# Performance work log

Hardware: AMD Instinct MI355X
Metric: run time of the kernel (lower is better)

The kernel has to match this reference:

```python
import jax, jax.numpy as jnp
import numpy as np

N = 10000
E = 160000
HEADS = 4
HC = 32      # hidden_channels
OC = 64      # out_channels
NG = 16      # n_goods
H1, H2 = 512, 256
NEG_SLOPE = 0.2


def setup_inputs() -> dict:
    key = jax.random.key(0)
    ks = jax.random.split(key, 32)
    rn = lambda k, s, sc=0.05: (jax.random.normal(k, s, jnp.float32) * sc)
    inp = {
        "x": jax.random.normal(ks[0], (N, 63), jnp.float32),
        "next_demand": jax.random.normal(ks[1], (N, 1), jnp.float32),
        "edge_index": jax.random.randint(ks[2], (2, E), 0, N),
        "eps": jax.random.normal(ks[3], (E, NG), jnp.float32),
        "Wl3": rn(ks[4], (HEADS * HC, 64)), "Wr3": rn(ks[5], (HEADS * HC, 64)),
        "att3": rn(ks[6], (HEADS, HC)), "b3": rn(ks[7], (HEADS * HC,)),
        # gat4: 128 -> 64, 1 head, mean
        "Wl4": rn(ks[8], (OC, HEADS * HC)), "Wr4": rn(ks[9], (OC, HEADS * HC)),
        "att4": rn(ks[10], (1, OC)), "b4": rn(ks[11], (OC,)),
        "Wl1": rn(ks[12], (HEADS * HC, OC)), "Wr1": rn(ks[13], (HEADS * HC, OC)),
        "att1": rn(ks[14], (HEADS, HC)), "b1": rn(ks[15], (HEADS * HC,)),
        # gat2: 128 -> 64, 1 head, mean
        "Wl2": rn(ks[16], (OC, HEADS * HC)), "Wr2": rn(ks[17], (OC, HEADS * HC)),
        "att2": rn(ks[18], (1, OC)), "b2": rn(ks[19], (OC,)),
        # MLP head: 256 -> 512 -> 256 -> n_goods (mu, std)
        "W_fc": rn(ks[20], (H1, OC * 4)), "b_fc": rn(ks[21], (H1,)),
        "W_fc1": rn(ks[22], (H2, H1)), "b_fc1": rn(ks[23], (H2,)),
        "W_mu": rn(ks[24], (NG, H2)), "b_mu": rn(ks[25], (NG,)),
        "W_std": rn(ks[26], (NG, H2)), "b_std": rn(ks[27], (NG,)),
    }
    return inp


def gatv2(x, src, dst, n, Wl, Wr, att, bias, heads, oc, concat):
    # GATv2Conv: e = a . LeakyReLU(Wl x_src + Wr x_dst), softmax over dst neighborhoods
    xl = (x @ Wl.T).reshape(n, heads, oc)
    xr = (x @ Wr.T).reshape(n, heads, oc)
    e = jax.nn.leaky_relu(xl[src] + xr[dst], NEG_SLOPE)        # [E', H, C]
    score = jnp.einsum('ehc,hc->eh', e, att)                   # [E', H]
    m = jax.ops.segment_max(score, dst, num_segments=n)        # stable segment softmax
    ex = jnp.exp(score - m[dst])
    den = jax.ops.segment_sum(ex, dst, num_segments=n)
    alpha = ex / (den[dst] + 1e-16)
    out = jax.ops.segment_sum(alpha[:, :, None] * xl[src], dst, num_segments=n)
    out = out.reshape(n, heads * oc) if concat else out.mean(axis=1)
    return out + bias


def reference(x, next_demand, edge_index, eps,
              Wl3, Wr3, att3, b3, Wl4, Wr4, att4, b4,
              Wl1, Wr1, att1, b1, Wl2, Wr2, att2, b2,
              W_fc, b_fc, W_fc1, b_fc1, W_mu, b_mu, W_std, b_std):
    n = x.shape[0]
    lrelu = lambda v: jax.nn.leaky_relu(v, NEG_SLOPE)
    loop = jnp.arange(n)
    # forward edges + self loops (PyG GATv2Conv add_self_loops=True)
    src = jnp.concatenate([edge_index[0], loop])
    dst = jnp.concatenate([edge_index[1], loop])
    # reverse edges + self loops
    rsrc = jnp.concatenate([edge_index[1], loop])
    rdst = jnp.concatenate([edge_index[0], loop])

    h = jnp.concatenate([x, next_demand.reshape(n, -1)], axis=1)   # [N, 64]
    xb = lrelu(gatv2(h, rsrc, rdst, n, Wl3, Wr3, att3, b3, HEADS, HC, True))
    xb = lrelu(gatv2(xb, rsrc, rdst, n, Wl4, Wr4, att4, b4, 1, OC, False))
    xf = lrelu(gatv2(xb, src, dst, n, Wl1, Wr1, att1, b1, HEADS, HC, True))
    xf = lrelu(gatv2(xf, src, dst, n, Wl2, Wr2, att2, b2, 1, OC, False))

    s = jnp.concatenate([xf, xb], axis=1)                          # [N, 128]
    se = jnp.concatenate([s[edge_index[0]], s[edge_index[1]]], axis=1)  # [E, 256]
    se = jax.nn.relu(se @ W_fc.T + b_fc)
    se = jax.nn.relu(se @ W_fc1.T + b_fc1)
    mu = se @ W_mu.T + b_mu
    std = jax.nn.softplus(se @ W_std.T + b_std)

    action = mu + std * eps                                        # rsample
    log2pi = jnp.log(2.0 * jnp.pi).astype(mu.dtype)
    lp = -0.5 * ((action - mu) / std) ** 2 - jnp.log(std) - 0.5 * log2pi
    log_prob = lp.reshape(1, -1).sum(-1, keepdims=True)            # num_graphs=1
    real_action = jnp.tanh(action)
    real_log_prob = log_prob - jnp.log(1.0 - real_action ** 2 + 1e-7).reshape(1, -1).sum(-1, keepdims=True)
    return (real_action.reshape(-1), real_log_prob)
```

## Files before the change

kernel.cpp:

```cpp
#include <hip/hip_runtime.h>
#include <hip/hip_bf16.h>
#include <math.h>

typedef __attribute__((ext_vector_type(8))) short short8;
typedef __attribute__((ext_vector_type(4))) float floatx4;

#define LRELU_S 0.2f
#define HALF_LOG_2PI 0.91893853320467274178f

__device__ __forceinline__ short f2bf(float f) {
  union { float f; unsigned u; } x; x.f = f;
  unsigned r = x.u + 0x7FFFu + ((x.u >> 16) & 1u);
  return (short)(r >> 16);
}
__device__ __forceinline__ float lrelu(float v) { return v > 0.f ? v : LRELU_S * v; }

__global__ __launch_bounds__(256) void k_concat_h(const float* __restrict__ x,
    const float* __restrict__ nd, float* __restrict__ h, int total) {
  int t = blockIdx.x * 256 + threadIdx.x;
  if (t >= total) return;
  int n = t >> 6, j = t & 63;
  h[t] = (j < 63) ? x[n * 63 + j] : nd[n];
}

__global__ __launch_bounds__(256) void k_deg(const int* __restrict__ ei,
    int* __restrict__ degF, int* __restrict__ degR, int E) {
  int e = blockIdx.x * 256 + threadIdx.x;
  if (e >= E) return;
  int a = ei[e], b = ei[E + e];
  atomicAdd(degF + b, 1);
  atomicAdd(degR + a, 1);
}

__global__ __launch_bounds__(256) void k_scan2(const int* __restrict__ degF,
    int* __restrict__ startF, int* __restrict__ curF,
    const int* __restrict__ degR, int* __restrict__ startR, int* __restrict__ curR, int n) {
  const int* __restrict__ deg = blockIdx.x ? degR : degF;
  int* __restrict__ start = blockIdx.x ? startR : startF;
  int* __restrict__ cur   = blockIdx.x ? curR : curF;
  __shared__ int part[256];
  int chunk = (n + 255) / 256;
  int t = threadIdx.x;
  int lo = t * chunk, hi = min(lo + chunk, n);
  int s = 0;
  for (int i = lo; i < hi; i++) s += deg[i] + 1;
  part[t] = s;
  __syncthreads();
  if (t == 0) {
    int acc = 0;
    for (int i = 0; i < 256; i++) { int v = part[i]; part[i] = acc; acc += v; }
    start[n] = acc;
  }
  __syncthreads();
  int acc = part[t];
  for (int i = lo; i < hi; i++) {
    start[i] = acc; cur[i] = acc;
    acc += deg[i] + 1;
  }
}

__global__ __launch_bounds__(256) void k_scatter(const int* __restrict__ ei,
    int* __restrict__ curF, int* __restrict__ curR,
    int* __restrict__ csrF, int* __restrict__ csrR, int E) {
  int e = blockIdx.x * 256 + threadIdx.x;
  if (e >= E) return;
  int a = ei[e], b = ei[E + e];
  int pf = atomicAdd(curF + b, 1); csrF[pf] = a;
  int pr = atomicAdd(curR + a, 1); csrR[pr] = b;
}

__global__ __launch_bounds__(256) void k_self(const int* __restrict__ startF,
    const int* __restrict__ startR, int* __restrict__ csrF, int* __restrict__ csrR, int n) {
  int d = blockIdx.x * 256 + threadIdx.x;
  if (d >= n) return;
  csrF[startF[d + 1] - 1] = d;
  csrR[startR[d + 1] - 1] = d;
}

template<int K, int F>
__global__ __launch_bounds__(256) void k_node_gemm(const float* __restrict__ in,
    const float* __restrict__ Wl, const float* __restrict__ Wr,
    float* __restrict__ xl, float* __restrict__ xr, int n) {
  __shared__ float sx[32][K + 1];
  const int row0 = blockIdx.x * 32;
  const float* __restrict__ W = blockIdx.y ? Wr : Wl;
  float* __restrict__ out = blockIdx.y ? xr : xl;
  const int tid = threadIdx.x;
  for (int i = tid; i < 32 * K; i += 256) {
    int r = i / K, c = i - r * K;
    sx[r][c] = (row0 + r < n) ? in[(size_t)(row0 + r) * K + c] : 0.f;
  }
  __syncthreads();
  const int nl = tid & 31;
  const int fg = tid >> 5;
  const int row = row0 + nl;
  if (row >= n) return;
  constexpr int FP = F / 8;
  for (int i = 0; i < FP; i++) {
    int f = fg * FP + i;
    const float* __restrict__ wrow = W + (size_t)f * K;
    float acc = 0.f;
    #pragma unroll
    for (int k = 0; k < K; k += 4) {
      float4 wv = *(const float4*)(wrow + k);
      acc += sx[nl][k] * wv.x + sx[nl][k + 1] * wv.y
           + sx[nl][k + 2] * wv.z + sx[nl][k + 3] * wv.w;
    }
    out[(size_t)row * F + f] = acc;
  }
}

template<int HF, int C>
__global__ __launch_bounds__(256) void k_gat_fused(const float* __restrict__ XL,
    const float* __restrict__ XR, const float* __restrict__ att,
    const float* __restrict__ bias, const int* __restrict__ start,
    const int* __restrict__ csr, float* __restrict__ out, int n) {
  constexpr int G = HF / 4;
  constexpr int DPB = 256 / G;
  int d = blockIdx.x * DPB + threadIdx.x / G;
  if (d >= n) return;
  int f4 = threadIdx.x & (G - 1);
  float4 xr = *(const float4*)(XR + (size_t)d * HF + f4 * 4);
  float4 av = *(const float4*)(att + f4 * 4);
  float4 bv = *(const float4*)(bias + f4 * 4);
  float m = -INFINITY, den = 0.f;
  float4 acc = {0.f, 0.f, 0.f, 0.f};
  int j1 = start[d + 1];
  for (int j = start[d]; j < j1; j++) {
    int s = csr[j];
    float4 xl = *(const float4*)(XL + (size_t)s * HF + f4 * 4);
    float e0 = xl.x + xr.x; e0 = e0 > 0.f ? e0 : LRELU_S * e0;
    float e1 = xl.y + xr.y; e1 = e1 > 0.f ? e1 : LRELU_S * e1;
    float e2 = xl.z + xr.z; e2 = e2 > 0.f ? e2 : LRELU_S * e2;
    float e3 = xl.w + xr.w; e3 = e3 > 0.f ? e3 : LRELU_S * e3;
    float partial = av.x * e0 + av.y * e1 + av.z * e2 + av.w * e3;
    #pragma unroll
    for (int o = C / 8; o > 0; o >>= 1) partial += __shfl_xor(partial, o, 64);
    float sc = partial;
    float mn = fmaxf(m, sc);
    float scale = expf(m - mn);
    float p = expf(sc - mn);
    den = den * scale + p;
    acc.x = acc.x * scale + p * xl.x;
    acc.y = acc.y * scale + p * xl.y;
    acc.z = acc.z * scale + p * xl.z;
    acc.w = acc.w * scale + p * xl.w;
    m = mn;
  }
  float inv = 1.f / (den + 1e-16f);
  float4 o4;
  o4.x = lrelu(acc.x * inv + bv.x);
  o4.y = lrelu(acc.y * inv + bv.y);
  o4.z = lrelu(acc.z * inv + bv.z);
  o4.w = lrelu(acc.w * inv + bv.w);
  *(float4*)(out + (size_t)d * HF + f4 * 4) = o4;
}

__global__ __launch_bounds__(256) void k_concat_s(const float* __restrict__ XF,
    const float* __restrict__ XB, short* __restrict__ SBF, int total) {
  int t = blockIdx.x * 256 + threadIdx.x;
  if (t >= total) return;
  int n = t >> 7, j = t & 127;
  float v = (j < 64) ? XF[n * 64 + j] : XB[n * 64 + (j - 64)];
  SBF[t] = f2bf(v);
}

__global__ __launch_bounds__(256) void k_wconv(const float* __restrict__ Wfc,
    const float* __restrict__ Wfc1, const float* __restrict__ Wmu,
    const float* __restrict__ Wstd, short* __restrict__ WBF) {
  int t = blockIdx.x * 256 + threadIdx.x;
  if (t >= 270336) return;
  int tile = t >> 9, pos = t & 511;
  int lane = pos >> 3, j = pos & 7;
  int lr = lane & 15, lg = lane >> 4;
  float v;
  if (tile < 256) {
    int nt = tile >> 3, kk = tile & 7;
    v = Wfc[(nt * 16 + lr) * 256 + kk * 32 + lg * 8 + j];
  } else if (tile < 512) {
    int t2 = tile - 256;
    int nt = t2 >> 4, kk = t2 & 15;
    v = Wfc1[(nt * 16 + lr) * 512 + kk * 32 + lg * 8 + j];
  } else {
    int t3 = tile - 512;
    int nt = t3 >> 3, kk = t3 & 7;
    int r = nt * 16 + lr;
    int col = kk * 32 + lg * 8 + j;
    v = (r < 16) ? Wmu[r * 256 + col] : Wstd[(r - 16) * 256 + col];
  }
  WBF[t] = f2bf(v);
}

__device__ __forceinline__ short8 lds_frag(const char* base, int row, int strideB, int k0, int lg) {
  int off = row * strideB + (((k0 * 2) + lg * 16) ^ ((row & 7) << 4));
  return *(const short8*)(base + off);
}

__global__ __launch_bounds__(512, 4) void k_head(
    const short* __restrict__ SBF, const short* __restrict__ WBF,
    const int* __restrict__ ei, const float* __restrict__ epsg,
    const float* __restrict__ b_fc, const float* __restrict__ b_fc1,
    const float* __restrict__ b_mu, const float* __restrict__ b_std,
    float* __restrict__ out, double* __restrict__ LP, int E) {
  __shared__ __align__(16) char lX[32768];
  __shared__ __align__(16) char cbuf[16384];
  float* lMS  = (float*)cbuf;
  float* lred = (float*)(cbuf + 8192);

  const int tid = threadIdx.x;
  const int eg0 = blockIdx.x * 64;

  for (int q = tid; q < 2048; q += 512) {
    int le = q >> 5, c = q & 31;
    int eg = eg0 + le;
    int node = (c < 16) ? ei[eg] : ei[E + eg];
    const short* srcp = SBF + (size_t)node * 128 + (c & 15) * 8;
    int4 v = *(const int4*)srcp;
    int col = (c * 16) ^ ((le & 7) << 4);
    *(int4*)(lX + le * 512 + col) = v;
  }
  __syncthreads();

  const int w = tid >> 6, lane = tid & 63;
  const int lr = lane & 15, lg = lane >> 4;
  const floatx4 zero = {0.f, 0.f, 0.f, 0.f};

  floatx4 acc2[2][4];
  #pragma unroll
  for (int a = 0; a < 2; a++)
    #pragma unroll
    for (int b = 0; b < 4; b++) acc2[a][b] = zero;

  for (int c = 0; c < 4; c++) {
    floatx4 acc1[4];
    #pragma unroll
    for (int mi = 0; mi < 4; mi++) acc1[mi] = zero;
    for (int kk = 0; kk < 8; kk++) {
      int tile = (c * 8 + w) * 8 + kk;
      short8 b = *(const short8*)(WBF + tile * 512 + lane * 8);
      #pragma unroll
      for (int mi = 0; mi < 4; mi++) {
        short8 a = lds_frag(lX, mi * 16 + lr, 512, kk * 32, lg);
        acc1[mi] = __builtin_amdgcn_mfma_f32_16x16x32_bf16(a, b, acc1[mi], 0, 0, 0);
      }
    }
    __syncthreads();
    {
      int cl = w * 16 + lr;
      float bv = b_fc[c * 128 + cl];
      #pragma unroll
      for (int mi = 0; mi < 4; mi++)
        #pragma unroll
        for (int j = 0; j < 4; j++) {
          int row = mi * 16 + lg * 4 + j;
          float v = acc1[mi][j] + bv;
          v = v > 0.f ? v : 0.f;
          *(short*)(cbuf + row * 256 + ((cl * 2) ^ ((row & 7) << 4))) = f2bf(v);
        }
    }
    __syncthreads();

    for (int kk2 = 0; kk2 < 4; kk2++) {
      short8 a[4];
      #pragma unroll
      for (int mi = 0; mi < 4; mi++) a[mi] = lds_frag(cbuf, mi * 16 + lr, 256, kk2 * 32, lg);
      #pragma unroll
      for (int ni2 = 0; ni2 < 2; ni2++) {
        int tile = 256 + (2 * w + ni2) * 16 + (c * 4 + kk2);
        short8 b = *(const short8*)(WBF + tile * 512 + lane * 8);
        #pragma unroll
        for (int mi = 0; mi < 4; mi++)
          acc2[ni2][mi] = __builtin_amdgcn_mfma_f32_16x16x32_bf16(a[mi], b, acc2[ni2][mi], 0, 0, 0);
      }
    }
  }
  __syncthreads();

  #pragma unroll
  for (int ni2 = 0; ni2 < 2; ni2++) {
    int n = (2 * w + ni2) * 16 + lr;
    float bv = b_fc1[n];
    #pragma unroll
    for (int mi = 0; mi < 4; mi++)
      #pragma unroll
      for (int j = 0; j < 4; j++) {
        int row = mi * 16 + lg * 4 + j;
        float v = acc2[ni2][mi][j] + bv;
        v = v > 0.f ? v : 0.f;
        *(short*)(lX + row * 512 + ((n * 2) ^ ((row & 7) << 4))) = f2bf(v);
      }
  }
  __syncthreads();

  {
    const int mfr = w >> 1, nfr = w & 1;
    floatx4 acc3 = zero;
    for (int kk = 0; kk < 8; kk++) {
      short8 a = lds_frag(lX, mfr * 16 + lr, 512, kk * 32, lg);
      int tile = 512 + nfr * 8 + kk;
      short8 b = *(const short8*)(WBF + tile * 512 + lane * 8);
      acc3 = __builtin_amdgcn_mfma_f32_16x16x32_bf16(a, b, acc3, 0, 0, 0);
    }
    int coln = nfr * 16 + lr;
    float bv = (coln < 16) ? b_mu[coln] : b_std[coln - 16];
    #pragma unroll
    for (int j = 0; j < 4; j++) {
      int row = mfr * 16 + lg * 4 + j;
      lMS[row * 32 + coln] = acc3[j] + bv;
    }
  }
  __syncthreads();

  float lpsum = 0.f;
  #pragma unroll
  for (int it = 0; it < 2; it++) {
    int idx = tid + it * 512;
    int m = idx >> 4, g = idx & 15;
    float mu = lMS[m * 32 + g];
    float sr = lMS[m * 32 + 16 + g];
    float sd = (sr > 20.f) ? sr : log1pf(expf(sr));
    int eg = eg0 + m;
    float ep = epsg[(size_t)eg * 16 + g];
    float action = mu + sd * ep;
    float ra = tanhf(action);
    out[(size_t)eg * 16 + g] = ra;
    lpsum += -0.5f * ep * ep - logf(sd) - HALF_LOG_2PI - logf(1.f - ra * ra + 1e-7f);
  }
  #pragma unroll
  for (int o = 32; o > 0; o >>= 1) lpsum += __shfl_xor(lpsum, o, 64);
  if (lane == 0) lred[w] = lpsum;
  __syncthreads();
  if (tid == 0) {
    double ssum = 0.0;
    #pragma unroll
    for (int i = 0; i < 8; i++) ssum += (double)lred[i];
    atomicAdd(LP, ssum);
  }
}

__global__ void k_finalize(const double* __restrict__ LP, float* __restrict__ out, int pos) {
  out[pos] = (float)(*LP);
}

extern "C" void kernel_launch(void* const* d_in, const int* in_sizes, int n_in,
                              void* d_out, int out_size, void* d_ws, size_t ws_size,
                              hipStream_t stream) {
  const float* x    = (const float*)d_in[0];
  const float* nd   = (const float*)d_in[1];
  const int*   ei   = (const int*)d_in[2];
  const float* epsg = (const float*)d_in[3];
  const float* Wl3 = (const float*)d_in[4];  const float* Wr3 = (const float*)d_in[5];
  const float* att3 = (const float*)d_in[6]; const float* b3 = (const float*)d_in[7];
  const float* Wl4 = (const float*)d_in[8];  const float* Wr4 = (const float*)d_in[9];
  const float* att4 = (const float*)d_in[10]; const float* b4 = (const float*)d_in[11];
  const float* Wl1 = (const float*)d_in[12]; const float* Wr1 = (const float*)d_in[13];
  const float* att1 = (const float*)d_in[14]; const float* b1 = (const float*)d_in[15];
  const float* Wl2 = (const float*)d_in[16]; const float* Wr2 = (const float*)d_in[17];
  const float* att2 = (const float*)d_in[18]; const float* b2 = (const float*)d_in[19];
  const float* W_fc  = (const float*)d_in[20]; const float* b_fc  = (const float*)d_in[21];
  const float* W_fc1 = (const float*)d_in[22]; const float* b_fc1 = (const float*)d_in[23];
  const float* W_mu  = (const float*)d_in[24]; const float* b_mu  = (const float*)d_in[25];
  const float* W_std = (const float*)d_in[26]; const float* b_std = (const float*)d_in[27];

  const int N = in_sizes[0] / 63;
  const int E = in_sizes[2] / 2;
  const int E2 = E + N;
  const size_t NN = (size_t)N;

  char* base = (char*)d_ws;
  auto alloc = [&](size_t bytes) { char* p = base; base += (bytes + 15) & ~(size_t)15; return p; };

  float* bufA = (float*)alloc(NN * 128 * 4);
  float* bufB = (float*)alloc(NN * 128 * 4);
  float* XL   = (float*)alloc(NN * 128 * 4);
  float* XR   = (float*)alloc(NN * 128 * 4);
  float* XBp  = (float*)alloc(NN * 64 * 4);
  float* XFp  = (float*)alloc(NN * 64 * 4);
  int* degF   = (int*)alloc(NN * 4);
  int* degR   = (int*)alloc(NN * 4);
  int* curF   = (int*)alloc(NN * 4);
  int* curR   = (int*)alloc(NN * 4);
  int* startF = (int*)alloc((NN + 1) * 4);
  int* startR = (int*)alloc((NN + 1) * 4);
  int* csrF   = (int*)alloc((size_t)E2 * 4);
  int* csrR   = (int*)alloc((size_t)E2 * 4);
  double* LPp = (double*)alloc(8);
  short* SBF  = (short*)alloc(NN * 128 * 2);
  short* WBF  = (short*)alloc(270336 * 2);

  auto nb = [](int total) { return (total + 255) / 256; };

  hipMemsetAsync(degF, 0, NN * 4, stream);
  hipMemsetAsync(degR, 0, NN * 4, stream);
  k_deg<<<nb(E), 256, 0, stream>>>(ei, degF, degR, E);
  k_scan2<<<2, 256, 0, stream>>>(degF, startF, curF, degR, startR, curR, N);
  k_scatter<<<nb(E), 256, 0, stream>>>(ei, curF, curR, csrF, csrR, E);
  k_self<<<nb(N), 256, 0, stream>>>(startF, startR, csrF, csrR, N);

  k_concat_h<<<nb(N * 64), 256, 0, stream>>>(x, nd, bufA, N * 64);
  k_wconv<<<nb(270336), 256, 0, stream>>>(W_fc, W_fc1, W_mu, W_std, WBF);

  { dim3 g((N + 31) / 32, 2);
    k_node_gemm<64, 128><<<g, 256, 0, stream>>>(bufA, Wl3, Wr3, XL, XR, N); }
  k_gat_fused<128, 32><<<(N + 7) / 8, 256, 0, stream>>>(XL, XR, att3, b3, startR, csrR, bufB, N);

  { dim3 g((N + 31) / 32, 2);
    k_node_gemm<128, 64><<<g, 256, 0, stream>>>(bufB, Wl4, Wr4, XL, XR, N); }
  k_gat_fused<64, 64><<<(N + 15) / 16, 256, 0, stream>>>(XL, XR, att4, b4, startR, csrR, XBp, N);

  { dim3 g((N + 31) / 32, 2);
    k_node_gemm<64, 128><<<g, 256, 0, stream>>>(XBp, Wl1, Wr1, XL, XR, N); }
  k_gat_fused<128, 32><<<(N + 7) / 8, 256, 0, stream>>>(XL, XR, att1, b1, startF, csrF, bufB, N);

  { dim3 g((N + 31) / 32, 2);
    k_node_gemm<128, 64><<<g, 256, 0, stream>>>(bufB, Wl2, Wr2, XL, XR, N); }
  k_gat_fused<64, 64><<<(N + 15) / 16, 256, 0, stream>>>(XL, XR, att2, b2, startF, csrF, XFp, N);

  k_concat_s<<<nb(N * 128), 256, 0, stream>>>(XFp, XBp, SBF, N * 128);
  hipMemsetAsync(LPp, 0, 8, stream);
  k_head<<<E / 64, 512, 0, stream>>>(SBF, WBF, ei, epsg, b_fc, b_fc1, b_mu, b_std,
                                     (float*)d_out, LPp, E);
  k_finalize<<<1, 1, 0, stream>>>(LPp, (float*)d_out, E * 16);
}
```

Baseline: 495.5 us.

## Fuse concat/self-loop kernels, use fast math intrinsics, change LDS swizzle

Folds the self-loop CSR writes into the scan kernel and the bf16 concat into the last GAT kernels, which write bf16 straight into the head's input buffer. This removes two launches and one intermediate buffer round trip. Precise expf/logf/tanhf/divide are replaced by fast intrinsics and hardware reciprocal, and the head's LDS XOR swizzle pattern changes to a different bank mapping. Fast math loosens accuracy, notably the 1-tanh^2 term inside the log-prob sum.

```diff
diff --git a/kernel.cpp b/kernel.cpp
--- a/kernel.cpp
+++ b/kernel.cpp
@@ -14,6 +14,14 @@
   return (short)(r >> 16);
 }
 __device__ __forceinline__ float lrelu(float v) { return v > 0.f ? v : LRELU_S * v; }
+__device__ __forceinline__ float frcp(float v) { return __builtin_amdgcn_rcpf(v); }
+__device__ __forceinline__ float ftanh(float x) {
+  float e = __expf(2.f * x);
+  return 1.f - 2.f * frcp(e + 1.f);
+}
+__device__ __forceinline__ int swzb(int row) {
+  return ((((row >> 2) & 3) << 1) | (row & 1)) << 4;
+}
 
 __global__ __launch_bounds__(256) void k_concat_h(const float* __restrict__ x,
     const float* __restrict__ nd, float* __restrict__ h, int total) {
@@ -33,11 +41,13 @@
 }
 
 __global__ __launch_bounds__(256) void k_scan2(const int* __restrict__ degF,
-    int* __restrict__ startF, int* __restrict__ curF,
-    const int* __restrict__ degR, int* __restrict__ startR, int* __restrict__ curR, int n) {
+    int* __restrict__ startF, int* __restrict__ curF, int* __restrict__ csrF,
+    const int* __restrict__ degR, int* __restrict__ startR, int* __restrict__ curR,
+    int* __restrict__ csrR, int n) {
   const int* __restrict__ deg = blockIdx.x ? degR : degF;
   int* __restrict__ start = blockIdx.x ? startR : startF;
   int* __restrict__ cur   = blockIdx.x ? curR : curF;
+  int* __restrict__ csr   = blockIdx.x ? csrR : csrF;
   __shared__ int part[256];
   int chunk = (n + 255) / 256;
   int t = threadIdx.x;
@@ -56,6 +66,7 @@
   for (int i = lo; i < hi; i++) {
     start[i] = acc; cur[i] = acc;
     acc += deg[i] + 1;
+    csr[acc - 1] = i;
   }
 }
 
@@ -67,14 +78,6 @@
   int a = ei[e], b = ei[E + e];
   int pf = atomicAdd(curF + b, 1); csrF[pf] = a;
   int pr = atomicAdd(curR + a, 1); csrR[pr] = b;
-}
-
-__global__ __launch_bounds__(256) void k_self(const int* __restrict__ startF,
-    const int* __restrict__ startR, int* __restrict__ csrF, int* __restrict__ csrR, int n) {
-  int d = blockIdx.x * 256 + threadIdx.x;
-  if (d >= n) return;
-  csrF[startF[d + 1] - 1] = d;
-  csrR[startR[d + 1] - 1] = d;
 }
 
 template<int K, int F>
@@ -110,11 +113,12 @@
   }
 }
 
-template<int HF, int C>
+template<int HF, int C, int OM>
 __global__ __launch_bounds__(256) void k_gat_fused(const float* __restrict__ XL,
     const float* __restrict__ XR, const float* __restrict__ att,
     const float* __restrict__ bias, const int* __restrict__ start,
-    const int* __restrict__ csr, float* __restrict__ out, int n) {
+    const int* __restrict__ csr, float* __restrict__ out,
+    short* __restrict__ sout, int scol, int n) {
   constexpr int G = HF / 4;
   constexpr int DPB = 256 / G;
   int d = blockIdx.x * DPB + threadIdx.x / G;
@@ -138,8 +142,8 @@
     for (int o = C / 8; o > 0; o >>= 1) partial += __shfl_xor(partial, o, 64);
     float sc = partial;
     float mn = fmaxf(m, sc);
-    float scale = expf(m - mn);
-    float p = expf(sc - mn);
+    float scale = __expf(m - mn);
+    float p = __expf(sc - mn);
     den = den * scale + p;
     acc.x = acc.x * scale + p * xl.x;
     acc.y = acc.y * scale + p * xl.y;
@@ -147,22 +151,19 @@
     acc.w = acc.w * scale + p * xl.w;
     m = mn;
   }
-  float inv = 1.f / (den + 1e-16f);
+  float inv = frcp(den + 1e-16f);
   float4 o4;
   o4.x = lrelu(acc.x * inv + bv.x);
   o4.y = lrelu(acc.y * inv + bv.y);
   o4.z = lrelu(acc.z * inv + bv.z);
   o4.w = lrelu(acc.w * inv + bv.w);
-  *(float4*)(out + (size_t)d * HF + f4 * 4) = o4;
-}
-
-__global__ __launch_bounds__(256) void k_concat_s(const float* __restrict__ XF,
-    const float* __restrict__ XB, short* __restrict__ SBF, int total) {
-  int t = blockIdx.x * 256 + threadIdx.x;
-  if (t >= total) return;
-  int n = t >> 7, j = t & 127;
-  float v = (j < 64) ? XF[n * 64 + j] : XB[n * 64 + (j - 64)];
-  SBF[t] = f2bf(v);
+  if (OM != 2) *(float4*)(out + (size_t)d * HF + f4 * 4) = o4;
+  if (OM != 0) {
+    union { short s[4]; int2 v; } u;
+    u.s[0] = f2bf(o4.x); u.s[1] = f2bf(o4.y);
+    u.s[2] = f2bf(o4.z); u.s[3] = f2bf(o4.w);
+    *(int2*)(sout + (size_t)d * 128 + scol + f4 * 4) = u.v;
+  }
 }
 
 __global__ __launch_bounds__(256) void k_wconv(const float* __restrict__ Wfc,
@@ -192,7 +193,7 @@
 }
 
 __device__ __forceinline__ short8 lds_frag(const char* base, int row, int strideB, int k0, int lg) {
-  int off = row * strideB + (((k0 * 2) + lg * 16) ^ ((row & 7) << 4));
+  int off = row * strideB + (((k0 * 2) + lg * 16) ^ swzb(row));
   return *(const short8*)(base + off);
 }
 
@@ -216,7 +217,7 @@
     int node = (c < 16) ? ei[eg] : ei[E + eg];
     const short* srcp = SBF + (size_t)node * 128 + (c & 15) * 8;
     int4 v = *(const int4*)srcp;
-    int col = (c * 16) ^ ((le & 7) << 4);
+    int col = (c * 16) ^ swzb(le);
     *(int4*)(lX + le * 512 + col) = v;
   }
   __syncthreads();
@@ -255,7 +256,7 @@
           int row = mi * 16 + lg * 4 + j;
           float v = acc1[mi][j] + bv;
           v = v > 0.f ? v : 0.f;
-          *(short*)(cbuf + row * 256 + ((cl * 2) ^ ((row & 7) << 4))) = f2bf(v);
+          *(short*)(cbuf + row * 256 + ((cl * 2) ^ swzb(row))) = f2bf(v);
         }
     }
     __syncthreads();
@@ -287,7 +288,7 @@
         int row = mi * 16 + lg * 4 + j;
         float v = acc2[ni2][mi][j] + bv;
         v = v > 0.f ? v : 0.f;
-        *(short*)(lX + row * 512 + ((n * 2) ^ ((row & 7) << 4))) = f2bf(v);
+        *(short*)(lX + row * 512 + ((n * 2) ^ swzb(row))) = f2bf(v);
       }
   }
   __syncthreads();
@@ -318,13 +319,13 @@
     int m = idx >> 4, g = idx & 15;
     float mu = lMS[m * 32 + g];
     float sr = lMS[m * 32 + 16 + g];
-    float sd = (sr > 20.f) ? sr : log1pf(expf(sr));
+    float sd = (sr > 20.f) ? sr : __logf(1.f + __expf(sr));
     int eg = eg0 + m;
     float ep = epsg[(size_t)eg * 16 + g];
     float action = mu + sd * ep;
-    float ra = tanhf(action);
+    float ra = ftanh(action);
     out[(size_t)eg * 16 + g] = ra;
-    lpsum += -0.5f * ep * ep - logf(sd) - HALF_LOG_2PI - logf(1.f - ra * ra + 1e-7f);
+    lpsum += -0.5f * ep * ep - __logf(sd) - HALF_LOG_2PI - __logf(1.f - ra * ra + 1e-7f);
   }
   #pragma unroll
   for (int o = 32; o > 0; o >>= 1) lpsum += __shfl_xor(lpsum, o, 64);
@@ -375,7 +376,6 @@
   float* XL   = (float*)alloc(NN * 128 * 4);
   float* XR   = (float*)alloc(NN * 128 * 4);
   float* XBp  = (float*)alloc(NN * 64 * 4);
-  float* XFp  = (float*)alloc(NN * 64 * 4);
   int* degF   = (int*)alloc(NN * 4);
   int* degR   = (int*)alloc(NN * 4);
   int* curF   = (int*)alloc(NN * 4);
@@ -390,33 +390,30 @@
 
   auto nb = [](int total) { return (total + 255) / 256; };
 
-  hipMemsetAsync(degF, 0, NN * 4, stream);
-  hipMemsetAsync(degR, 0, NN * 4, stream);
+  hipMemsetAsync(degF, 0, NN * 8, stream);
   k_deg<<<nb(E), 256, 0, stream>>>(ei, degF, degR, E);
-  k_scan2<<<2, 256, 0, stream>>>(degF, startF, curF, degR, startR, curR, N);
+  k_scan2<<<2, 256, 0, stream>>>(degF, startF, curF, csrF, degR, startR, curR, csrR, N);
   k_scatter<<<nb(E), 256, 0, stream>>>(ei, curF, curR, csrF, csrR, E);
-  k_self<<<nb(N), 256, 0, stream>>>(startF, startR, csrF, csrR, N);
 
   k_concat_h<<<nb(N * 64), 256, 0, stream>>>(x, nd, bufA, N * 64);
   k_wconv<<<nb(270336), 256, 0, stream>>>(W_fc, W_fc1, W_mu, W_std, WBF);
 
   { dim3 g((N + 31) / 32, 2);
     k_node_gemm<64, 128><<<g, 256, 0, stream>>>(bufA, Wl3, Wr3, XL, XR, N); }
-  k_gat_fused<128, 32><<<(N + 7) / 8, 256, 0, stream>>>(XL, XR, att3, b3, startR, csrR, bufB, N);
+  k_gat_fused<128, 32, 0><<<(N + 7) / 8, 256, 0, stream>>>(XL, XR, att3, b3, startR, csrR, bufB, nullptr, 0, N);
 
   { dim3 g((N + 31) / 32, 2);
     k_node_gemm<128, 64><<<g, 256, 0, stream>>>(bufB, Wl4, Wr4, XL, XR, N); }
-  k_gat_fused<64, 64><<<(N + 15) / 16, 256, 0, stream>>>(XL, XR, att4, b4, startR, csrR, XBp, N);
+  k_gat_fused<64, 64, 1><<<(N + 15) / 16, 256, 0, stream>>>(XL, XR, att4, b4, startR, csrR, XBp, SBF, 64, N);
 
   { dim3 g((N + 31) / 32, 2);
     k_node_gemm<64, 128><<<g, 256, 0, stream>>>(XBp, Wl1, Wr1, XL, XR, N); }
-  k_gat_fused<128, 32><<<(N + 7) / 8, 256, 0, stream>>>(XL, XR, att1, b1, startF, csrF, bufB, N);
+  k_gat_fused<128, 32, 0><<<(N + 7) / 8, 256, 0, stream>>>(XL, XR, att1, b1, startF, csrF, bufB, nullptr, 0, N);
 
   { dim3 g((N + 31) / 32, 2);
     k_node_gemm<128, 64><<<g, 256, 0, stream>>>(bufB, Wl2, Wr2, XL, XR, N); }
-  k_gat_fused<64, 64><<<(N + 15) / 16, 256, 0, stream>>>(XL, XR, att2, b2, startF, csrF, XFp, N);
-
-  k_concat_s<<<nb(N * 128), 256, 0, stream>>>(XFp, XBp, SBF, N * 128);
+  k_gat_fused<64, 64, 2><<<(N + 15) / 16, 256, 0, stream>>>(XL, XR, att2, b2, startF, csrF, nullptr, SBF, 0, N);
+
   hipMemsetAsync(LPp, 0, 8, stream);
   k_head<<<E / 64, 512, 0, stream>>>(SBF, WBF, ei, epsg, b_fc, b_fc1, b_mu, b_std,
                                      (float*)d_out, LPp, E);
```

Measured after the change: 479.6 us. 1.03x faster.
